# Kernel optimization log

Measured on AMD Instinct MI355X. Metric: run time of the kernel, lower is better.

## Reference

```python
import jax, jax.numpy as jnp
import numpy as np

N_NODES = 50000
N_EDGES = 500000
HIDDEN = 64
HEADS = 8
VOCAB = 40000
N_GRAPHS = 512


def setup_inputs() -> dict:
    key = jax.random.key(0)
    ks = jax.random.split(key, 16)
    s = 0.05  # keep attention logits in a sane range
    emb = jax.random.normal(ks[0], (VOCAB + 1, HIDDEN), jnp.float32) * s
    emb = emb.at[0].set(0.0)  # padding_idx=0
    return {
        'x': jax.random.randint(ks[1], (N_NODES,), 0, VOCAB + 1),
        'edge_index': jax.random.randint(ks[2], (2, N_EDGES), 0, N_NODES),
        'batch': jnp.sort(jax.random.randint(ks[3], (N_NODES,), 0, N_GRAPHS)),
        'emb': emb,
        'W1': jax.random.normal(ks[4], (HIDDEN, HEADS * HIDDEN), jnp.float32) * s,
        'a_src1': jax.random.normal(ks[5], (HEADS, HIDDEN), jnp.float32) * s,
        'a_dst1': jax.random.normal(ks[6], (HEADS, HIDDEN), jnp.float32) * s,
        'b1': jax.random.normal(ks[7], (HEADS * HIDDEN,), jnp.float32) * s,
        'W2': jax.random.normal(ks[8], (HEADS * HIDDEN, HIDDEN), jnp.float32) * s,
        'a_src2': jax.random.normal(ks[9], (1, HIDDEN), jnp.float32) * s,
        'a_dst2': jax.random.normal(ks[10], (1, HIDDEN), jnp.float32) * s,
        'b2': jax.random.normal(ks[11], (HIDDEN,), jnp.float32) * s,
        'Wp': jax.random.normal(ks[12], (HIDDEN, VOCAB), jnp.float32) * s,
        'bp': jax.random.normal(ks[13], (VOCAB,), jnp.float32) * s,
    }


def _gat_conv(h, src, dst, W, a_src, a_dst, b, heads, out_c, concat):
    # PyG GATConv (eval mode, self-loops already appended by caller).
    n = h.shape[0]
    hp = (h @ W).reshape(n, heads, out_c)              # [N, H, C]
    s_src = jnp.einsum('nhc,hc->nh', hp, a_src)        # per-node src score
    s_dst = jnp.einsum('nhc,hc->nh', hp, a_dst)        # per-node dst score
    logits = jax.nn.leaky_relu(s_src[src] + s_dst[dst], negative_slope=0.2)  # [E, H]
    # segment softmax over destination-node neighborhoods
    m = jax.ops.segment_max(logits, dst, num_segments=n)
    m = jnp.where(jnp.isfinite(m), m, 0.0)
    e = jnp.exp(logits - m[dst])
    denom = jax.ops.segment_sum(e, dst, num_segments=n)
    alpha = e / (denom[dst] + 1e-16)                   # [E, H]
    msgs = hp[src] * alpha[:, :, None]                 # [E, H, C]
    out = jax.ops.segment_sum(msgs, dst, num_segments=n)
    out = out.reshape(n, heads * out_c) if concat else out.mean(axis=1)
    return out + b


def reference(x, edge_index, batch, emb, W1, a_src1, a_dst1, b1, W2, a_src2, a_dst2, b2, Wp, bp):
    n = x.shape[0]
    loop = jnp.arange(n)
    src = jnp.concatenate([edge_index[0], loop])  # add_self_loops=True
    dst = jnp.concatenate([edge_index[1], loop])
    h = emb[x]                                     # embedding lookup [N, 64]
    h = jax.nn.elu(_gat_conv(h, src, dst, W1, a_src1, a_dst1, b1, HEADS, HIDDEN, True))
    h = _gat_conv(h, src, dst, W2, a_src2, a_dst2, b2, 1, HIDDEN, False)
    pooled = jax.ops.segment_sum(h, batch, num_segments=N_GRAPHS)  # global_add_pool
    return pooled @ Wp + bp
```

## Files before the change

### kernel.cpp

```cpp
#include <hip/hip_runtime.h>
#include <hip/hip_bf16.h>
#include <hip/hip_fp16.h>

#define N_NODESC 50000
#define N_EDGESC 500000
#define E_TOT    (N_EDGESC + N_NODESC)
#define HID      64
#define HEADS_C  8
#define F1       (HEADS_C * HID)
#define VOCAB_C  40000
#define N_GR     512
#define SCAN_B   196

typedef __attribute__((ext_vector_type(8))) short bf16x8;
typedef __attribute__((ext_vector_type(4))) float f32x4;
typedef __attribute__((ext_vector_type(8))) _Float16 half8;

__device__ __forceinline__ float lrelu(float x) { return x > 0.f ? x : 0.2f * x; }
__device__ __forceinline__ float bf2f(unsigned short u) {
  return __uint_as_float(((unsigned int)u) << 16);
}
__device__ __forceinline__ unsigned short f2bf(float f) {
  unsigned int u = __float_as_uint(f);
  unsigned int r = (u + 0x7fffu + ((u >> 16) & 1u)) >> 16;
  return (unsigned short)r;
}
__device__ __forceinline__ unsigned short f2h(float f) {
  __half h = __float2half(f);
  union { __half h; unsigned short u; } c; c.h = h; return c.u;
}
__device__ __forceinline__ __half2 as_h2(unsigned int v) {
  union { unsigned int u; __half2 h; } c; c.u = v; return c.h;
}
__device__ __forceinline__ unsigned int h2u(__half2 h) {
  union { __half2 h; unsigned int u; } c; c.h = h; return c.u;
}

__global__ void k_zero(int* __restrict__ deg, float* __restrict__ pooled) {
  int i = blockIdx.x * 256 + threadIdx.x;
  if (i < N_NODESC) deg[i] = 0;
  if (i < N_GR * HID) pooled[i] = 0.f;
}

__global__ void k_deg(const int* __restrict__ ei, int* __restrict__ deg,
                      int* __restrict__ eslot) {
  int e = blockIdx.x * blockDim.x + threadIdx.x;
  if (e >= E_TOT) return;
  int dst = (e < N_EDGESC) ? ei[N_EDGESC + e] : (e - N_EDGESC);
  eslot[e] = atomicAdd(&deg[dst], 1);
}

__global__ __launch_bounds__(256) void k_scan1(const int* __restrict__ deg,
                                               int* __restrict__ rowtmp,
                                               int* __restrict__ partials) {
  __shared__ int sh[256];
  int b = blockIdx.x, t = threadIdx.x, i = b * 256 + t;
  int d = (i < N_NODESC) ? deg[i] : 0;
  sh[t] = d;
  __syncthreads();
  for (int o = 1; o < 256; o <<= 1) {
    int v = (t >= o) ? sh[t - o] : 0;
    __syncthreads();
    sh[t] += v;
    __syncthreads();
  }
  if (i < N_NODESC) rowtmp[i] = sh[t];
  if (t == 255) partials[b] = sh[255];
}

__global__ __launch_bounds__(256) void k_scan3(const int* __restrict__ deg,
                                               const int* __restrict__ rowtmp,
                                               const int* __restrict__ partials,
                                               int* __restrict__ rowstart) {
  __shared__ int wsum[4];
  int b = blockIdx.x, t = threadIdx.x;
  int acc = 0;
  for (int i = t; i < b; i += 256) acc += partials[i];
#pragma unroll
  for (int o = 32; o; o >>= 1) acc += __shfl_xor(acc, o);
  if ((t & 63) == 0) wsum[t >> 6] = acc;
  __syncthreads();
  int base = wsum[0] + wsum[1] + wsum[2] + wsum[3];
  int i = b * 256 + t;
  if (i < N_NODESC) rowstart[i] = base + rowtmp[i] - deg[i];
  if (i == N_NODESC - 1) rowstart[N_NODESC] = base + rowtmp[i];
}

__global__ void k_scatter(const int* __restrict__ ei, const int* __restrict__ rowstart,
                          const int* __restrict__ eslot, int* __restrict__ esrc) {
  int e = blockIdx.x * blockDim.x + threadIdx.x;
  if (e >= E_TOT) return;
  int src, dst;
  if (e < N_EDGESC) { src = ei[e]; dst = ei[N_EDGESC + e]; }
  else { src = dst = e - N_EDGESC; }
  esrc[rowstart[dst] + eslot[e]] = src;
}

__global__ __launch_bounds__(512) void k_prepwconv(const float* __restrict__ W1,
                                                   const float* __restrict__ as1,
                                                   const float* __restrict__ ad1,
                                                   const float* __restrict__ W2,
                                                   const float* __restrict__ as2,
                                                   const float* __restrict__ ad2,
                                                   const float* __restrict__ Wp,
                                                   float* __restrict__ w2sv,
                                                   float* __restrict__ w2dv,
                                                   unsigned short* __restrict__ waB,
                                                   unsigned short* __restrict__ w1bT,
                                                   unsigned short* __restrict__ w2bT,
                                                   unsigned short* __restrict__ wpT) {
  __shared__ float ws[64][65];
  int b = blockIdx.x, t = threadIdx.x;
  if (b < 64) {
    int g = b * 512 + t;
    int c = g >> 6, k = g & 63;
    w1bT[g] = f2bf(W1[(size_t)k * F1 + c]);
  } else if (b < 128) {
    int idx = (b - 64) * 512 + t;
    int c = idx >> 9, k = idx & 511;
    w2bT[idx] = f2bf(W2[(size_t)k * HID + c]);
  } else if (b == 128) {
    int k = t >> 3, h = t & 7;
    float ss = 0.f, dd = 0.f;
    for (int c = 0; c < 64; ++c) {
      float w = W1[k * F1 + h * 64 + c];
      ss += w * as1[h * 64 + c];
      dd += w * ad1[h * 64 + c];
    }
    waB[h * 64 + k] = f2bf(ss);
    waB[(8 + h) * 64 + k] = f2bf(dd);
    float s2 = 0.f, d2 = 0.f;
    for (int c = 0; c < 64; ++c) {
      float w = W2[t * 64 + c];
      s2 += w * as2[c];
      d2 += w * ad2[c];
    }
    w2sv[t] = s2;
    w2dv[t] = d2;
  } else {
    int v0 = (b - 129) * 64;
#pragma unroll
    for (int rep = 0; rep < 8; ++rep) {
      int idx = rep * 512 + t;
      int k = idx >> 6, v = idx & 63;
      ws[k][v] = Wp[(size_t)k * VOCAB_C + v0 + v];
    }
    __syncthreads();
#pragma unroll
    for (int rep = 0; rep < 8; ++rep) {
      int idx = rep * 512 + t;
      int v = idx >> 6, k = idx & 63;
      wpT[(size_t)(v0 + v) * 64 + k] = f2bf(ws[k][v]);
    }
  }
}

__global__ __launch_bounds__(256) void k_embed(const int* __restrict__ x,
                                               const float* __restrict__ emb,
                                               const unsigned short* __restrict__ waB,
                                               unsigned short* __restrict__ hf,
                                               float* __restrict__ s1s,
                                               float* __restrict__ s1d) {
  int t = threadIdx.x;
  int w = t >> 6, lane = t & 63;
  int lrow = lane & 15, lq = lane >> 4;
  int n0 = blockIdx.x * 64 + w * 16;
  if (n0 >= N_NODESC) return;
  int node = n0 + lrow;
  const float* er = emb + (size_t)x[node] * 64;
  float4 f0 = *reinterpret_cast<const float4*>(er + lq * 8);
  float4 f1 = *reinterpret_cast<const float4*>(er + lq * 8 + 4);
  float4 f2 = *reinterpret_cast<const float4*>(er + 32 + lq * 8);
  float4 f3 = *reinterpret_cast<const float4*>(er + 32 + lq * 8 + 4);
  bf16x8 a0, a1;
  a0[0] = (short)f2bf(f0.x); a0[1] = (short)f2bf(f0.y);
  a0[2] = (short)f2bf(f0.z); a0[3] = (short)f2bf(f0.w);
  a0[4] = (short)f2bf(f1.x); a0[5] = (short)f2bf(f1.y);
  a0[6] = (short)f2bf(f1.z); a0[7] = (short)f2bf(f1.w);
  a1[0] = (short)f2bf(f2.x); a1[1] = (short)f2bf(f2.y);
  a1[2] = (short)f2bf(f2.z); a1[3] = (short)f2bf(f2.w);
  a1[4] = (short)f2bf(f3.x); a1[5] = (short)f2bf(f3.y);
  a1[6] = (short)f2bf(f3.z); a1[7] = (short)f2bf(f3.w);
  half8 h0, h1;
  h0[0] = (_Float16)f0.x; h0[1] = (_Float16)f0.y;
  h0[2] = (_Float16)f0.z; h0[3] = (_Float16)f0.w;
  h0[4] = (_Float16)f1.x; h0[5] = (_Float16)f1.y;
  h0[6] = (_Float16)f1.z; h0[7] = (_Float16)f1.w;
  h1[0] = (_Float16)f2.x; h1[1] = (_Float16)f2.y;
  h1[2] = (_Float16)f2.z; h1[3] = (_Float16)f2.w;
  h1[4] = (_Float16)f3.x; h1[5] = (_Float16)f3.y;
  h1[6] = (_Float16)f3.z; h1[7] = (_Float16)f3.w;
  *reinterpret_cast<half8*>(&hf[(size_t)node * 64 + lq * 8]) = h0;
  *reinterpret_cast<half8*>(&hf[(size_t)node * 64 + 32 + lq * 8]) = h1;
  const bf16x8* brow = reinterpret_cast<const bf16x8*>(waB + lrow * 64 + lq * 8);
  f32x4 acc = {};
  acc = __builtin_amdgcn_mfma_f32_16x16x32_bf16(a0, brow[0], acc, 0, 0, 0);
  acc = __builtin_amdgcn_mfma_f32_16x16x32_bf16(a1, brow[4], acc, 0, 0, 0);
  float* dst = (lrow < 8) ? s1s : s1d;
  int h = lrow & 7;
#pragma unroll
  for (int r = 0; r < 4; ++r)
    dst[(size_t)(n0 + lq * 4 + r) * 8 + h] = acc[r];
}

__global__ __launch_bounds__(256) void k_agg1(const int* __restrict__ rowstart,
                                              const int* __restrict__ esrc,
                                              const unsigned short* __restrict__ hf,
                                              const float* __restrict__ s1s,
                                              const float* __restrict__ s1d,
                                              unsigned short* __restrict__ agg8) {
  int n = blockIdx.x * 4 + (threadIdx.x >> 6);
  int L = threadIdx.x & 63;
  int eh = L >> 3;
  int hh = L & 7;
  int myh = L >> 3;
  const int fc = (L & 7) * 8;
  int r0 = rowstart[n], dg = rowstart[n + 1] - r0;
  float sdst = s1d[n * 8 + hh];
  __half2 ac0 = __float2half2_rn(0.f), ac1 = ac0, ac2 = ac0, ac3 = ac0;
  float dsum = 0.f;
  for (int base = 0; base < dg; base += 8) {
    int i = base + eh;
    float p = 0.f;
    int s = 0;
    if (i < dg) {
      s = esrc[r0 + i];
      p = __expf(lrelu(s1s[s * 8 + hh] + sdst));
    }
    dsum += p;
    int cnt = min(8, dg - base);
    for (int j = 0; j < cnt; ++j) {
      float pj = __shfl(p, (j << 3) | myh);
      int sj = __shfl(s, j << 3);
      uint4 u = *reinterpret_cast<const uint4*>(&hf[(size_t)sj * 64 + fc]);
      __half2 p2 = __float2half2_rn(pj);
      ac0 = __hfma2(as_h2(u.x), p2, ac0);
      ac1 = __hfma2(as_h2(u.y), p2, ac1);
      ac2 = __hfma2(as_h2(u.z), p2, ac2);
      ac3 = __hfma2(as_h2(u.w), p2, ac3);
    }
  }
  dsum += __shfl_xor(dsum, 8);
  dsum += __shfl_xor(dsum, 16);
  dsum += __shfl_xor(dsum, 32);
  float inv = 1.f / (__shfl(dsum, myh) + 1e-16f);
  float2 v0 = __half22float2(ac0);
  float2 v1 = __half22float2(ac1);
  float2 v2 = __half22float2(ac2);
  float2 v3 = __half22float2(ac3);
  uint4 ov;
  ov.x = (unsigned int)f2bf(v0.x * inv) | ((unsigned int)f2bf(v0.y * inv) << 16);
  ov.y = (unsigned int)f2bf(v1.x * inv) | ((unsigned int)f2bf(v1.y * inv) << 16);
  ov.z = (unsigned int)f2bf(v2.x * inv) | ((unsigned int)f2bf(v2.y * inv) << 16);
  ov.w = (unsigned int)f2bf(v3.x * inv) | ((unsigned int)f2bf(v3.y * inv) << 16);
  *reinterpret_cast<uint4*>(&agg8[(size_t)n * F1 + L * 8]) = ov;
}

__global__ __launch_bounds__(256) void k_hgemm(const unsigned short* __restrict__ agg8,
                                               const unsigned short* __restrict__ w1bT,
                                               const float* __restrict__ b1,
                                               unsigned short* __restrict__ h1b) {
  __shared__ unsigned short Ts[16][520];
  __shared__ float bs[512];
  int t = threadIdx.x;
  int n0 = blockIdx.x * 16;
  bs[t] = b1[t]; bs[t + 256] = b1[t + 256];
  int w = t >> 6, lane = t & 63;
  int lrow = lane & 15, lq = lane >> 4;
  const unsigned short* arow = agg8 + (size_t)(n0 + lrow) * F1;
  int h0 = 2 * w;
  bf16x8 a00 = *reinterpret_cast<const bf16x8*>(arow + h0 * 64 + lq * 8);
  bf16x8 a01 = *reinterpret_cast<const bf16x8*>(arow + h0 * 64 + 32 + lq * 8);
  bf16x8 a10 = *reinterpret_cast<const bf16x8*>(arow + (h0 + 1) * 64 + lq * 8);
  bf16x8 a11 = *reinterpret_cast<const bf16x8*>(arow + (h0 + 1) * 64 + 32 + lq * 8);
  int c0 = w * 128;
  f32x4 acc[8] = {};
#pragma unroll
  for (int ct = 0; ct < 8; ++ct) {
    int col = c0 + ct * 16 + lrow;
    const bf16x8* brow = reinterpret_cast<const bf16x8*>(w1bT + (size_t)col * 64 + lq * 8);
    if (ct < 4) {
      acc[ct] = __builtin_amdgcn_mfma_f32_16x16x32_bf16(a00, brow[0], acc[ct], 0, 0, 0);
      acc[ct] = __builtin_amdgcn_mfma_f32_16x16x32_bf16(a01, brow[4], acc[ct], 0, 0, 0);
    } else {
      acc[ct] = __builtin_amdgcn_mfma_f32_16x16x32_bf16(a10, brow[0], acc[ct], 0, 0, 0);
      acc[ct] = __builtin_amdgcn_mfma_f32_16x16x32_bf16(a11, brow[4], acc[ct], 0, 0, 0);
    }
  }
  __syncthreads();
#pragma unroll
  for (int ct = 0; ct < 8; ++ct) {
    int col = c0 + ct * 16 + lrow;
#pragma unroll
    for (int r = 0; r < 4; ++r) {
      float v = acc[ct][r] + bs[col];
      v = v > 0.f ? v : (__expf(v) - 1.f);
      Ts[lq * 4 + r][col] = f2bf(v);
    }
  }
  __syncthreads();
  for (int i = t; i < 1024; i += 256) {
    int r = i >> 6, c16 = i & 63;
    reinterpret_cast<uint4*>(&h1b[(size_t)(n0 + r) * F1])[c16] =
        *reinterpret_cast<const uint4*>(&Ts[r][c16 * 8]);
  }
}

__global__ __launch_bounds__(256) void k_gemm2(const unsigned short* __restrict__ h1b,
                                               const unsigned short* __restrict__ w2bT,
                                               const float* __restrict__ w2sv,
                                               const float* __restrict__ w2dv,
                                               unsigned short* __restrict__ hp2h,
                                               float* __restrict__ s2s,
                                               float* __restrict__ s2d) {
  __shared__ float wsv[512], wdv[512];
  int t = threadIdx.x;
  for (int i = t; i < 512; i += 256) { wsv[i] = w2sv[i]; wdv[i] = w2dv[i]; }
  __syncthreads();
  int w = t >> 6, lane = t & 63;
  int lrow = lane & 15, lq = lane >> 4;
  int nb = blockIdx.x * 64 + w * 16;
  if (nb >= N_NODESC) return;
  f32x4 acc[4] = {};
  float ssp = 0.f, ddp = 0.f;
  const unsigned short* arowp = h1b + (size_t)(nb + lrow) * F1;
#pragma unroll 4
  for (int kq = 0; kq < 16; ++kq) {
    int kbase = kq * 32 + lq * 8;
    bf16x8 a = *reinterpret_cast<const bf16x8*>(arowp + kbase);
#pragma unroll
    for (int i = 0; i < 8; ++i) {
      float f = bf2f((unsigned short)a[i]);
      ssp += f * wsv[kbase + i];
      ddp += f * wdv[kbase + i];
    }
#pragma unroll
    for (int ct = 0; ct < 4; ++ct) {
      bf16x8 b = *reinterpret_cast<const bf16x8*>(w2bT + (size_t)(ct * 16 + lrow) * F1 + kbase);
      acc[ct] = __builtin_amdgcn_mfma_f32_16x16x32_bf16(a, b, acc[ct], 0, 0, 0);
    }
  }
  ssp += __shfl_xor(ssp, 16); ssp += __shfl_xor(ssp, 32);
  ddp += __shfl_xor(ddp, 16); ddp += __shfl_xor(ddp, 32);
  if (lane < 16) { s2s[nb + lane] = ssp; s2d[nb + lane] = ddp; }
#pragma unroll
  for (int ct = 0; ct < 4; ++ct) {
    int col = ct * 16 + lrow;
#pragma unroll
    for (int r = 0; r < 4; ++r)
      hp2h[(size_t)(nb + lq * 4 + r) * HID + col] = f2h(acc[ct][r]);
  }
}

__global__ __launch_bounds__(256) void k_agg2(const int* __restrict__ rowstart,
                                              const int* __restrict__ esrc,
                                              const unsigned short* __restrict__ hp2h,
                                              const float* __restrict__ s2s,
                                              const float* __restrict__ s2d,
                                              const float* __restrict__ b2,
                                              const int* __restrict__ batch,
                                              float* __restrict__ pooled) {
  int n = blockIdx.x * 4 + (threadIdx.x >> 6);
  int lane = threadIdx.x & 63;
  int half = lane >> 5;
  int fl = lane & 31;
  int r0 = rowstart[n], dg = rowstart[n + 1] - r0;
  float sdst = s2d[n];
  __half2 ac = __float2half2_rn(0.f);
  float dsum = 0.f;
  for (int base = 0; base < dg; base += 32) {
    int i = base + fl;
    float p = 0.f;
    int s = 0;
    if (i < dg) {
      s = esrc[r0 + i];
      p = __expf(lrelu(s2s[s] + sdst));
    }
    dsum += p;
    int cnt = min(32, dg - base);
    for (int j = 0; j < cnt; j += 2) {
      int jj = j + half;
      float pj = __shfl(p, jj, 32);
      int sj = __shfl(s, jj, 32);
      unsigned int hv = *reinterpret_cast<const unsigned int*>(&hp2h[(size_t)sj * 64 + fl * 2]);
      ac = __hfma2(as_h2(hv), __float2half2_rn(pj), ac);
    }
  }
#pragma unroll
  for (int o = 1; o < 32; o <<= 1) dsum += __shfl_xor(dsum, o);
  float inv = 1.f / (dsum + 1e-16f);
  unsigned int other = __shfl_xor(h2u(ac), 32);
  ac = __hadd2(ac, as_h2(other));
  float2 fv = __half22float2(ac);
  int f = 2 * fl + half;
  float o = (half ? fv.y : fv.x) * inv + b2[f];
  atomicAdd(&pooled[batch[n] * 64 + f], o);
}

__global__ __launch_bounds__(256) void k_final(const float* __restrict__ pooled,
                                               const unsigned short* __restrict__ wpT,
                                               const float* __restrict__ bp,
                                               float* __restrict__ out) {
  __shared__ unsigned short As[16][72];
  __shared__ float Cs[16][324];
  int t = threadIdx.x;
  int g0 = blockIdx.y * 16;
  int vb = blockIdx.x * 320;
  {
    int g = t >> 4, k4 = (t & 15) * 4;
    float4 pv = *reinterpret_cast<const float4*>(&pooled[(size_t)(g0 + g) * 64 + k4]);
    ushort4 u;
    u.x = f2bf(pv.x); u.y = f2bf(pv.y); u.z = f2bf(pv.z); u.w = f2bf(pv.w);
    *reinterpret_cast<ushort4*>(&As[g][k4]) = u;
  }
  __syncthreads();
  int w = t >> 6, lane = t & 63;
  int lrow = lane & 15, lq = lane >> 4;
  bf16x8 a0 = *reinterpret_cast<const bf16x8*>(&As[lrow][lq * 8]);
  bf16x8 a1 = *reinterpret_cast<const bf16x8*>(&As[lrow][32 + lq * 8]);
#pragma unroll
  for (int ct = 0; ct < 5; ++ct) {
    int cloc = (w * 5 + ct) * 16 + lrow;
    const bf16x8* brow = reinterpret_cast<const bf16x8*>(wpT + (size_t)(vb + cloc) * 64 + lq * 8);
    f32x4 acc = {};
    acc = __builtin_amdgcn_mfma_f32_16x16x32_bf16(a0, brow[0], acc, 0, 0, 0);
    acc = __builtin_amdgcn_mfma_f32_16x16x32_bf16(a1, brow[4], acc, 0, 0, 0);
#pragma unroll
    for (int r = 0; r < 4; ++r) Cs[lq * 4 + r][cloc] = acc[r];
  }
  __syncthreads();
  for (int i = t; i < 1280; i += 256) {
    int r = i / 80, c = i % 80;
    float4 cv = *reinterpret_cast<const float4*>(&Cs[r][c * 4]);
    float4 bv = *reinterpret_cast<const float4*>(&bp[vb + c * 4]);
    cv.x += bv.x; cv.y += bv.y; cv.z += bv.z; cv.w += bv.w;
    *reinterpret_cast<float4*>(&out[(size_t)(g0 + r) * VOCAB_C + vb + c * 4]) = cv;
  }
}

extern "C" void kernel_launch(void* const* d_in, const int* in_sizes, int n_in,
                              void* d_out, int out_size, void* d_ws, size_t ws_size,
                              hipStream_t stream) {
  const int*   x     = (const int*)d_in[0];
  const int*   ei    = (const int*)d_in[1];
  const int*   batch = (const int*)d_in[2];
  const float* emb   = (const float*)d_in[3];
  const float* W1    = (const float*)d_in[4];
  const float* as1   = (const float*)d_in[5];
  const float* ad1   = (const float*)d_in[6];
  const float* b1    = (const float*)d_in[7];
  const float* W2    = (const float*)d_in[8];
  const float* as2   = (const float*)d_in[9];
  const float* ad2   = (const float*)d_in[10];
  const float* b2    = (const float*)d_in[11];
  const float* Wp    = (const float*)d_in[12];
  const float* bp    = (const float*)d_in[13];
  float* out = (float*)d_out;

  char* ws = (char*)d_ws;
  size_t off = 0;
#define WS_ALLOC(T, name, bytes) T name = (T)(ws + off); off += (((size_t)(bytes)) + 255) & ~(size_t)255;
  WS_ALLOC(unsigned short*, hf,   (size_t)N_NODESC * HID * 2)
  WS_ALLOC(unsigned short*, agg8, (size_t)N_NODESC * F1 * 2)
  WS_ALLOC(unsigned short*, h1b,  (size_t)N_NODESC * F1 * 2)
  WS_ALLOC(unsigned short*, hp2h, (size_t)N_NODESC * HID * 2)
  WS_ALLOC(unsigned short*, w1bT, 512 * 64 * 2)
  WS_ALLOC(unsigned short*, w2bT, 64 * 512 * 2)
  WS_ALLOC(unsigned short*, wpT,  (size_t)VOCAB_C * HID * 2)
  WS_ALLOC(unsigned short*, waB,  16 * 64 * 2)
  WS_ALLOC(float*, s1s,  (size_t)N_NODESC * HEADS_C * 4)
  WS_ALLOC(float*, s1d,  (size_t)N_NODESC * HEADS_C * 4)
  WS_ALLOC(float*, s2s,  (size_t)N_NODESC * 4)
  WS_ALLOC(float*, s2d,  (size_t)N_NODESC * 4)
  WS_ALLOC(float*, pooled, (size_t)N_GR * HID * 4)
  WS_ALLOC(float*, w2sv, 512 * 4)
  WS_ALLOC(float*, w2dv, 512 * 4)
  WS_ALLOC(int*,   deg,      (size_t)N_NODESC * 4)
  WS_ALLOC(int*,   rowstart, (size_t)(N_NODESC + 1) * 4)
  WS_ALLOC(int*,   rowtmp,   (size_t)N_NODESC * 4)
  WS_ALLOC(int*,   partials, 256 * 4)
  WS_ALLOC(int*,   eslot,    (size_t)E_TOT * 4)
  WS_ALLOC(int*,   esrc,     (size_t)E_TOT * 4)
#undef WS_ALLOC
  (void)ws_size; (void)in_sizes; (void)n_in; (void)out_size;

  int ethreads = 256, eblocks = (E_TOT + 255) / 256;
  k_zero<<<SCAN_B, 256, 0, stream>>>(deg, pooled);
  k_deg<<<eblocks, ethreads, 0, stream>>>(ei, deg, eslot);
  k_scan1<<<SCAN_B, 256, 0, stream>>>(deg, rowtmp, partials);
  k_scan3<<<SCAN_B, 256, 0, stream>>>(deg, rowtmp, partials, rowstart);
  k_scatter<<<eblocks, ethreads, 0, stream>>>(ei, rowstart, eslot, esrc);
  k_prepwconv<<<129 + VOCAB_C / 64, 512, 0, stream>>>(
      W1, as1, ad1, W2, as2, ad2, Wp,
      w2sv, w2dv, waB, w1bT, w2bT, wpT);

  k_embed<<<(N_NODESC + 63) / 64, 256, 0, stream>>>(x, emb, waB, hf, s1s, s1d);
  k_agg1<<<N_NODESC / 4, 256, 0, stream>>>(rowstart, esrc, hf, s1s, s1d, agg8);
  k_hgemm<<<N_NODESC / 16, 256, 0, stream>>>(agg8, w1bT, b1, h1b);

  k_gemm2<<<(N_NODESC + 63) / 64, 256, 0, stream>>>(h1b, w2bT, w2sv, w2dv, hp2h, s2s, s2d);
  k_agg2<<<N_NODESC / 4, 256, 0, stream>>>(rowstart, esrc, hp2h, s2s, s2d, b2, batch, pooled);

  k_final<<<dim3(VOCAB_C / 320, N_GR / 16), 256, 0, stream>>>(pooled, wpT, bp, out);
}
```

Baseline: 267.0 us.

## Fuse layer-1 GEMM with layer-2 GEMM and restructure edge aggregation loops

Merges the layer-1 transform+ELU kernel with the layer-2 GEMM so the 50000x512 bf16 hidden activation stays in shared memory instead of being written to and re-read from global memory. The layer-2 attention scores are computed from the fp32 activations during the epilogue. Both aggregation kernels now have each 8-lane group process a different edge in parallel, with one vector load per edge instead of a serial per-edge loop, followed by cross-lane shuffle reductions. The agg1 rewrite keeps 32 half2 accumulators per thread and needs many reduction shuffles, which raises register pressure and may lower occupancy.

```diff
diff --git a/kernel.cpp b/kernel.cpp
--- a/kernel.cpp
+++ b/kernel.cpp
@@ -31,9 +31,6 @@
 }
 __device__ __forceinline__ __half2 as_h2(unsigned int v) {
   union { unsigned int u; __half2 h; } c; c.u = v; return c.h;
-}
-__device__ __forceinline__ unsigned int h2u(__half2 h) {
-  union { __half2 h; unsigned int u; } c; c.h = h; return c.u;
 }
 
 __global__ void k_zero(int* __restrict__ deg, float* __restrict__ pooled) {
@@ -213,41 +210,54 @@
   int L = threadIdx.x & 63;
   int eh = L >> 3;
   int hh = L & 7;
-  int myh = L >> 3;
-  const int fc = (L & 7) * 8;
+  int fc = L & 7;
   int r0 = rowstart[n], dg = rowstart[n + 1] - r0;
   float sdst = s1d[n * 8 + hh];
-  __half2 ac0 = __float2half2_rn(0.f), ac1 = ac0, ac2 = ac0, ac3 = ac0;
+  __half2 acc[8][4];
+#pragma unroll
+  for (int h = 0; h < 8; ++h)
+#pragma unroll
+    for (int k = 0; k < 4; ++k) acc[h][k] = __float2half2_rn(0.f);
   float dsum = 0.f;
   for (int base = 0; base < dg; base += 8) {
     int i = base + eh;
+    int s = 0;
     float p = 0.f;
-    int s = 0;
     if (i < dg) {
       s = esrc[r0 + i];
       p = __expf(lrelu(s1s[s * 8 + hh] + sdst));
     }
     dsum += p;
-    int cnt = min(8, dg - base);
-    for (int j = 0; j < cnt; ++j) {
-      float pj = __shfl(p, (j << 3) | myh);
-      int sj = __shfl(s, j << 3);
-      uint4 u = *reinterpret_cast<const uint4*>(&hf[(size_t)sj * 64 + fc]);
-      __half2 p2 = __float2half2_rn(pj);
-      ac0 = __hfma2(as_h2(u.x), p2, ac0);
-      ac1 = __hfma2(as_h2(u.y), p2, ac1);
-      ac2 = __hfma2(as_h2(u.z), p2, ac2);
-      ac3 = __hfma2(as_h2(u.w), p2, ac3);
+    uint4 u = *reinterpret_cast<const uint4*>(&hf[(size_t)s * 64 + fc * 8]);
+#pragma unroll
+    for (int h = 0; h < 8; ++h) {
+      __half2 p2 = __float2half2_rn(__shfl(p, (L & 56) | h));
+      acc[h][0] = __hfma2(as_h2(u.x), p2, acc[h][0]);
+      acc[h][1] = __hfma2(as_h2(u.y), p2, acc[h][1]);
+      acc[h][2] = __hfma2(as_h2(u.z), p2, acc[h][2]);
+      acc[h][3] = __hfma2(as_h2(u.w), p2, acc[h][3]);
     }
   }
   dsum += __shfl_xor(dsum, 8);
   dsum += __shfl_xor(dsum, 16);
   dsum += __shfl_xor(dsum, 32);
-  float inv = 1.f / (__shfl(dsum, myh) + 1e-16f);
-  float2 v0 = __half22float2(ac0);
-  float2 v1 = __half22float2(ac1);
-  float2 v2 = __half22float2(ac2);
-  float2 v3 = __half22float2(ac3);
+  float inv = 1.f / (__shfl(dsum, eh) + 1e-16f);
+#pragma unroll
+  for (int h = 0; h < 8; ++h)
+#pragma unroll
+    for (int k = 0; k < 4; ++k) {
+      acc[h][k] = __hadd2(acc[h][k], as_h2(__shfl_xor(__builtin_bit_cast(unsigned int, acc[h][k]), 8)));
+      acc[h][k] = __hadd2(acc[h][k], as_h2(__shfl_xor(__builtin_bit_cast(unsigned int, acc[h][k]), 16)));
+      acc[h][k] = __hadd2(acc[h][k], as_h2(__shfl_xor(__builtin_bit_cast(unsigned int, acc[h][k]), 32)));
+    }
+  __half2 sel0 = acc[0][0], sel1 = acc[0][1], sel2 = acc[0][2], sel3 = acc[0][3];
+#pragma unroll
+  for (int h = 1; h < 8; ++h)
+    if (eh == h) { sel0 = acc[h][0]; sel1 = acc[h][1]; sel2 = acc[h][2]; sel3 = acc[h][3]; }
+  float2 v0 = __half22float2(sel0);
+  float2 v1 = __half22float2(sel1);
+  float2 v2 = __half22float2(sel2);
+  float2 v3 = __half22float2(sel3);
   uint4 ov;
   ov.x = (unsigned int)f2bf(v0.x * inv) | ((unsigned int)f2bf(v0.y * inv) << 16);
   ov.y = (unsigned int)f2bf(v1.x * inv) | ((unsigned int)f2bf(v1.y * inv) << 16);
@@ -256,15 +266,23 @@
   *reinterpret_cast<uint4*>(&agg8[(size_t)n * F1 + L * 8]) = ov;
 }
 
-__global__ __launch_bounds__(256) void k_hgemm(const unsigned short* __restrict__ agg8,
-                                               const unsigned short* __restrict__ w1bT,
-                                               const float* __restrict__ b1,
-                                               unsigned short* __restrict__ h1b) {
+__global__ __launch_bounds__(256) void k_fused12(const unsigned short* __restrict__ agg8,
+                                                 const unsigned short* __restrict__ w1bT,
+                                                 const float* __restrict__ b1,
+                                                 const unsigned short* __restrict__ w2bT,
+                                                 const float* __restrict__ w2sv,
+                                                 const float* __restrict__ w2dv,
+                                                 unsigned short* __restrict__ hp2h,
+                                                 float* __restrict__ s2s,
+                                                 float* __restrict__ s2d) {
   __shared__ unsigned short Ts[16][520];
-  __shared__ float bs[512];
+  __shared__ float bs[512], wsv[512], wdv[512];
+  __shared__ float sredS[4][16], sredD[4][16];
   int t = threadIdx.x;
   int n0 = blockIdx.x * 16;
   bs[t] = b1[t]; bs[t + 256] = b1[t + 256];
+  wsv[t] = w2sv[t]; wsv[t + 256] = w2sv[t + 256];
+  wdv[t] = w2dv[t]; wdv[t + 256] = w2dv[t + 256];
   int w = t >> 6, lane = t & 63;
   int lrow = lane & 15, lq = lane >> 4;
   const unsigned short* arow = agg8 + (size_t)(n0 + lrow) * F1;
@@ -288,6 +306,7 @@
     }
   }
   __syncthreads();
+  float ssp[4] = {}, ddp[4] = {};
 #pragma unroll
   for (int ct = 0; ct < 8; ++ct) {
     int col = c0 + ct * 16 + lrow;
@@ -296,60 +315,38 @@
       float v = acc[ct][r] + bs[col];
       v = v > 0.f ? v : (__expf(v) - 1.f);
       Ts[lq * 4 + r][col] = f2bf(v);
-    }
+      ssp[r] += v * wsv[col];
+      ddp[r] += v * wdv[col];
+    }
+  }
+#pragma unroll
+  for (int r = 0; r < 4; ++r) {
+#pragma unroll
+    for (int o = 1; o < 16; o <<= 1) {
+      ssp[r] += __shfl_xor(ssp[r], o);
+      ddp[r] += __shfl_xor(ddp[r], o);
+    }
+  }
+  if (lrow == 0) {
+#pragma unroll
+    for (int r = 0; r < 4; ++r) { sredS[w][lq * 4 + r] = ssp[r]; sredD[w][lq * 4 + r] = ddp[r]; }
   }
   __syncthreads();
-  for (int i = t; i < 1024; i += 256) {
-    int r = i >> 6, c16 = i & 63;
-    reinterpret_cast<uint4*>(&h1b[(size_t)(n0 + r) * F1])[c16] =
-        *reinterpret_cast<const uint4*>(&Ts[r][c16 * 8]);
-  }
-}
-
-__global__ __launch_bounds__(256) void k_gemm2(const unsigned short* __restrict__ h1b,
-                                               const unsigned short* __restrict__ w2bT,
-                                               const float* __restrict__ w2sv,
-                                               const float* __restrict__ w2dv,
-                                               unsigned short* __restrict__ hp2h,
-                                               float* __restrict__ s2s,
-                                               float* __restrict__ s2d) {
-  __shared__ float wsv[512], wdv[512];
-  int t = threadIdx.x;
-  for (int i = t; i < 512; i += 256) { wsv[i] = w2sv[i]; wdv[i] = w2dv[i]; }
-  __syncthreads();
-  int w = t >> 6, lane = t & 63;
-  int lrow = lane & 15, lq = lane >> 4;
-  int nb = blockIdx.x * 64 + w * 16;
-  if (nb >= N_NODESC) return;
-  f32x4 acc[4] = {};
-  float ssp = 0.f, ddp = 0.f;
-  const unsigned short* arowp = h1b + (size_t)(nb + lrow) * F1;
+  f32x4 acc2 = {};
 #pragma unroll 4
   for (int kq = 0; kq < 16; ++kq) {
     int kbase = kq * 32 + lq * 8;
-    bf16x8 a = *reinterpret_cast<const bf16x8*>(arowp + kbase);
-#pragma unroll
-    for (int i = 0; i < 8; ++i) {
-      float f = bf2f((unsigned short)a[i]);
-      ssp += f * wsv[kbase + i];
-      ddp += f * wdv[kbase + i];
-    }
-#pragma unroll
-    for (int ct = 0; ct < 4; ++ct) {
-      bf16x8 b = *reinterpret_cast<const bf16x8*>(w2bT + (size_t)(ct * 16 + lrow) * F1 + kbase);
-      acc[ct] = __builtin_amdgcn_mfma_f32_16x16x32_bf16(a, b, acc[ct], 0, 0, 0);
-    }
-  }
-  ssp += __shfl_xor(ssp, 16); ssp += __shfl_xor(ssp, 32);
-  ddp += __shfl_xor(ddp, 16); ddp += __shfl_xor(ddp, 32);
-  if (lane < 16) { s2s[nb + lane] = ssp; s2d[nb + lane] = ddp; }
-#pragma unroll
-  for (int ct = 0; ct < 4; ++ct) {
-    int col = ct * 16 + lrow;
-#pragma unroll
-    for (int r = 0; r < 4; ++r)
-      hp2h[(size_t)(nb + lq * 4 + r) * HID + col] = f2h(acc[ct][r]);
-  }
+    bf16x8 a = *reinterpret_cast<const bf16x8*>(&Ts[lrow][kbase]);
+    bf16x8 b = *reinterpret_cast<const bf16x8*>(w2bT + (size_t)(w * 16 + lrow) * F1 + kbase);
+    acc2 = __builtin_amdgcn_mfma_f32_16x16x32_bf16(a, b, acc2, 0, 0, 0);
+  }
+  if (t < 16) {
+    s2s[n0 + t] = sredS[0][t] + sredS[1][t] + sredS[2][t] + sredS[3][t];
+    s2d[n0 + t] = sredD[0][t] + sredD[1][t] + sredD[2][t] + sredD[3][t];
+  }
+#pragma unroll
+  for (int r = 0; r < 4; ++r)
+    hp2h[(size_t)(n0 + lq * 4 + r) * HID + w * 16 + lrow] = f2h(acc2[r]);
 }
 
 __global__ __launch_bounds__(256) void k_agg2(const int* __restrict__ rowstart,
@@ -361,40 +358,55 @@
                                               const int* __restrict__ batch,
                                               float* __restrict__ pooled) {
   int n = blockIdx.x * 4 + (threadIdx.x >> 6);
-  int lane = threadIdx.x & 63;
-  int half = lane >> 5;
-  int fl = lane & 31;
+  int L = threadIdx.x & 63;
+  int eh = L >> 3;
+  int fc = L & 7;
   int r0 = rowstart[n], dg = rowstart[n + 1] - r0;
   float sdst = s2d[n];
-  __half2 ac = __float2half2_rn(0.f);
+  __half2 ac0 = __float2half2_rn(0.f), ac1 = ac0, ac2 = ac0, ac3 = ac0;
   float dsum = 0.f;
-  for (int base = 0; base < dg; base += 32) {
-    int i = base + fl;
+  for (int base = 0; base < dg; base += 8) {
+    int i = base + eh;
+    int s = 0;
     float p = 0.f;
-    int s = 0;
     if (i < dg) {
       s = esrc[r0 + i];
       p = __expf(lrelu(s2s[s] + sdst));
     }
     dsum += p;
-    int cnt = min(32, dg - base);
-    for (int j = 0; j < cnt; j += 2) {
-      int jj = j + half;
-      float pj = __shfl(p, jj, 32);
-      int sj = __shfl(s, jj, 32);
-      unsigned int hv = *reinterpret_cast<const unsigned int*>(&hp2h[(size_t)sj * 64 + fl * 2]);
-      ac = __hfma2(as_h2(hv), __float2half2_rn(pj), ac);
-    }
-  }
-#pragma unroll
-  for (int o = 1; o < 32; o <<= 1) dsum += __shfl_xor(dsum, o);
+    uint4 u = *reinterpret_cast<const uint4*>(&hp2h[(size_t)s * 64 + fc * 8]);
+    __half2 p2 = __float2half2_rn(p);
+    ac0 = __hfma2(as_h2(u.x), p2, ac0);
+    ac1 = __hfma2(as_h2(u.y), p2, ac1);
+    ac2 = __hfma2(as_h2(u.z), p2, ac2);
+    ac3 = __hfma2(as_h2(u.w), p2, ac3);
+  }
+  dsum += __shfl_xor(dsum, 8);
+  dsum += __shfl_xor(dsum, 16);
+  dsum += __shfl_xor(dsum, 32);
   float inv = 1.f / (dsum + 1e-16f);
-  unsigned int other = __shfl_xor(h2u(ac), 32);
-  ac = __hadd2(ac, as_h2(other));
-  float2 fv = __half22float2(ac);
-  int f = 2 * fl + half;
-  float o = (half ? fv.y : fv.x) * inv + b2[f];
-  atomicAdd(&pooled[batch[n] * 64 + f], o);
+#pragma unroll
+  for (int o = 8; o <= 32; o <<= 1) {
+    ac0 = __hadd2(ac0, as_h2(__shfl_xor(__builtin_bit_cast(unsigned int, ac0), o)));
+    ac1 = __hadd2(ac1, as_h2(__shfl_xor(__builtin_bit_cast(unsigned int, ac1), o)));
+    ac2 = __hadd2(ac2, as_h2(__shfl_xor(__builtin_bit_cast(unsigned int, ac2), o)));
+    ac3 = __hadd2(ac3, as_h2(__shfl_xor(__builtin_bit_cast(unsigned int, ac3), o)));
+  }
+  if (eh == 0) {
+    float2 f0 = __half22float2(ac0);
+    float2 f1 = __half22float2(ac1);
+    float2 f2 = __half22float2(ac2);
+    float2 f3 = __half22float2(ac3);
+    int gbase = batch[n] * 64 + fc * 8;
+    atomicAdd(&pooled[gbase + 0], f0.x * inv + b2[fc * 8 + 0]);
+    atomicAdd(&pooled[gbase + 1], f0.y * inv + b2[fc * 8 + 1]);
+    atomicAdd(&pooled[gbase + 2], f1.x * inv + b2[fc * 8 + 2]);
+    atomicAdd(&pooled[gbase + 3], f1.y * inv + b2[fc * 8 + 3]);
+    atomicAdd(&pooled[gbase + 4], f2.x * inv + b2[fc * 8 + 4]);
+    atomicAdd(&pooled[gbase + 5], f2.y * inv + b2[fc * 8 + 5]);
+    atomicAdd(&pooled[gbase + 6], f3.x * inv + b2[fc * 8 + 6]);
+    atomicAdd(&pooled[gbase + 7], f3.y * inv + b2[fc * 8 + 7]);
+  }
 }
 
 __global__ __launch_bounds__(256) void k_final(const float* __restrict__ pooled,
@@ -462,7 +474,6 @@
 #define WS_ALLOC(T, name, bytes) T name = (T)(ws + off); off += (((size_t)(bytes)) + 255) & ~(size_t)255;
   WS_ALLOC(unsigned short*, hf,   (size_t)N_NODESC * HID * 2)
   WS_ALLOC(unsigned short*, agg8, (size_t)N_NODESC * F1 * 2)
-  WS_ALLOC(unsigned short*, h1b,  (size_t)N_NODESC * F1 * 2)
   WS_ALLOC(unsigned short*, hp2h, (size_t)N_NODESC * HID * 2)
   WS_ALLOC(unsigned short*, w1bT, 512 * 64 * 2)
   WS_ALLOC(unsigned short*, w2bT, 64 * 512 * 2)
@@ -496,9 +507,8 @@
 
   k_embed<<<(N_NODESC + 63) / 64, 256, 0, stream>>>(x, emb, waB, hf, s1s, s1d);
   k_agg1<<<N_NODESC / 4, 256, 0, stream>>>(rowstart, esrc, hf, s1s, s1d, agg8);
-  k_hgemm<<<N_NODESC / 16, 256, 0, stream>>>(agg8, w1bT, b1, h1b);
-
-  k_gemm2<<<(N_NODESC + 63) / 64, 256, 0, stream>>>(h1b, w2bT, w2sv, w2dv, hp2h, s2s, s2d);
+  k_fused12<<<N_NODESC / 16, 256, 0, stream>>>(agg8, w1bT, b1, w2bT, w2sv, w2dv,
+                                               hp2h, s2s, s2d);
   k_agg2<<<N_NODESC / 4, 256, 0, stream>>>(rowstart, esrc, hp2h, s2s, s2d, b2, batch, pooled);
 
   k_final<<<dim3(VOCAB_C / 320, N_GR / 16), 256, 0, stream>>>(pooled, wpT, bp, out);
```

Result: slower. 375.0 us (+40.4%).
